# Kernel optimization log

Hardware: AMD Instinct MI355X
Metric: run time of the kernel (lower is better)

The kernel has to match this reference:

```python
import jax, jax.numpy as jnp
import numpy as np
import math

D_MODEL = 1024
D_STATE = 128
D_CONV = 4
EXPAND = 2
HEADDIM = 64
NGROUPS = 1
D_INNER = EXPAND * D_MODEL            # 2048
D_SSM = D_INNER                       # d_ssm defaults to d_inner
NHEADS = D_SSM // HEADDIM             # 32
CONV_DIM = D_SSM + 2 * NGROUPS * D_STATE   # 2304
D_IN_PROJ = 2 * D_INNER + 2 * NGROUPS * D_STATE + NHEADS  # 4384
EPS = 1e-5
DT_MIN, DT_MAX = 1e-3, 1e-1


def setup_inputs() -> dict:
    key = jax.random.key(0)
    ks = jax.random.split(key, 8)
    u = jax.random.normal(ks[0], (2, 4096, D_MODEL), dtype=jnp.float32)
    W_in = jax.random.normal(ks[1], (D_IN_PROJ, D_MODEL), dtype=jnp.float32) * 0.02
    conv_w = jax.random.normal(ks[2], (CONV_DIM, D_CONV), dtype=jnp.float32) * 0.1
    conv_b = jnp.zeros((CONV_DIM,), dtype=jnp.float32)
    # dt_bias init as in the module: inv-softplus of dt ~ logU(dt_min, dt_max)
    dt = jnp.exp(jax.random.uniform(ks[3], (NHEADS,)) * (math.log(DT_MAX) - math.log(DT_MIN)) + math.log(DT_MIN))
    dt_bias = dt + jnp.log(-jnp.expm1(-dt))
    A_log = jnp.log(jax.random.uniform(ks[4], (NHEADS,), minval=1.0, maxval=16.0))
    D = jnp.ones((NHEADS,), dtype=jnp.float32)
    norm_w = jnp.ones((D_SSM,), dtype=jnp.float32)
    W_out = jax.random.normal(ks[5], (D_MODEL, D_INNER), dtype=jnp.float32) * 0.02
    return {"u": u, "W_in": W_in, "conv_w": conv_w, "conv_b": conv_b,
            "dt_bias": dt_bias, "A_log": A_log, "D": D, "norm_w": norm_w, "W_out": W_out}


def _mamba2_forward(u, W_in, conv_w, conv_b, dt_bias, A_log, D, norm_w, W_out):
    b, L, _ = u.shape
    zxbcdt = jnp.einsum('bld,ed->ble', u, W_in)  # (b, L, D_IN_PROJ)
    z = zxbcdt[..., :D_SSM]
    xBC = zxbcdt[..., D_SSM:D_SSM + CONV_DIM]
    dt = zxbcdt[..., D_SSM + CONV_DIM:]                     # (b, L, H)
    dt = jax.nn.softplus(dt + dt_bias)                      # (b, L, H)

    # causal depthwise conv1d + SiLU (channel-last, kernel width D_CONV)
    xp = jnp.pad(xBC, ((0, 0), (D_CONV - 1, 0), (0, 0)))
    conv = conv_b
    for w in range(D_CONV):
        conv = conv + xp[:, w:w + L, :] * conv_w[:, w]
    xBC = jax.nn.silu(conv)

    x = xBC[..., :D_SSM].reshape(b, L, NHEADS, HEADDIM)     # (b, L, H, P)
    B = xBC[..., D_SSM:D_SSM + D_STATE]                     # (b, L, N), ngroups=1
    C = xBC[..., D_SSM + D_STATE:]                          # (b, L, N)

    A = -jnp.exp(A_log)                                     # (H,)
    dA = jnp.exp(dt * A)                                    # (b, L, H)
    dtx = dt[..., None] * x                                 # (b, L, H, P)

    # selective state-space scan over time: h_t = h_{t-1}*dA_t + dt_t*x_t (x) B_t
    def step(h, inp):
        dA_t, dtx_t, B_t, C_t = inp                        # (b,H), (b,H,P), (b,N), (b,N)
        h = h * dA_t[:, :, None, None] + jnp.einsum('bhp,bn->bhpn', dtx_t, B_t)
        y_t = jnp.einsum('bhpn,bn->bhp', h, C_t)
        return h, y_t

    h0 = jnp.zeros((b, NHEADS, HEADDIM, D_STATE), dtype=u.dtype)
    inputs = (jnp.moveaxis(dA, 1, 0), jnp.moveaxis(dtx, 1, 0),
              jnp.moveaxis(B, 1, 0), jnp.moveaxis(C, 1, 0))
    _, y = jax.lax.scan(step, h0, inputs)                   # (L, b, H, P)
    y = jnp.moveaxis(y, 0, 1) + x * D[None, None, :, None]  # D skip per head
    y = y.reshape(b, L, D_SSM)

    # gated RMSNorm (norm_before_gate=False): normalize(y * silu(z)) * weight
    g = y * jax.nn.silu(z)
    g = g * jax.lax.rsqrt(jnp.mean(g * g, axis=-1, keepdims=True) + EPS) * norm_w
    return jnp.einsum('ble,de->bld', g, W_out)              # (b, L, D_MODEL)


def reference(u, W_in, conv_w, conv_b, dt_bias, A_log, D, norm_w, W_out):
    return _mamba2_forward(u, W_in, conv_w, conv_b, dt_bias, A_log, D, norm_w, W_out)
```

## Files before the change

### kernel.cpp

```cpp
#include <hip/hip_runtime.h>
#include <hip/hip_bf16.h>
#include <cstdint>

#define BB     2
#define LSEQ   4096
#define DM     1024
#define DSSM   2048
#define NH     32
#define HD     64
#define DS     128
#define NPROJ  4384
#define NPAD   4480
#define CONVD  2304
#define ROWS   (BB*LSEQ)
#define CHUNK  128
#define NCH    (LSEQ/CHUNK)
#define NBHC   (BB*NH*NCH)

typedef __bf16 bf16x8 __attribute__((ext_vector_type(8)));
typedef float  f32x4  __attribute__((ext_vector_type(4)));
typedef float  f32x16 __attribute__((ext_vector_type(16)));

__device__ __forceinline__ __bf16 to_bf(float f) {
    __hip_bfloat16 h = __float2bfloat16(f);
    return *(__bf16*)&h;
}

__device__ __forceinline__ void direct_load16(const void* gp, void* lp) {
    typedef const __attribute__((address_space(1))) unsigned int* gptr_t;
    typedef __attribute__((address_space(3))) unsigned int* lptr_t;
    __builtin_amdgcn_global_load_lds((gptr_t)(uintptr_t)gp,
                                     (lptr_t)(unsigned int)(uintptr_t)lp,
                                     16, 0, 0);
}

#define N1 ((size_t)ROWS * DM)
#define N2 ((size_t)NPAD * DM)
#define N3 ((size_t)DM * DSSM)
#define NREAL ((size_t)NPROJ * DM)

__global__ __launch_bounds__(256) void convert_all(const float* __restrict__ u,
                                                   const float* __restrict__ W_in,
                                                   const float* __restrict__ W_out,
                                                   __hip_bfloat16* __restrict__ ub,
                                                   __hip_bfloat16* __restrict__ winb,
                                                   __hip_bfloat16* __restrict__ woutb) {
    size_t i4 = ((size_t)blockIdx.x * 256 + threadIdx.x) * 4;
    const float* src;
    __hip_bfloat16* dst;
    size_t j;
    if (i4 < N1) { src = u; dst = ub; j = i4; }
    else if (i4 < N1 + N2) {
        j = i4 - N1;
        if (j >= NREAL) {
            ushort4 z = {0, 0, 0, 0};
            *(ushort4*)&winb[j] = z;
            return;
        }
        src = W_in; dst = winb;
    } else { src = W_out; dst = woutb; j = i4 - N1 - N2; }
    float4 v = *(const float4*)&src[j];
    __hip_bfloat16 o[4] = {__float2bfloat16(v.x), __float2bfloat16(v.y),
                           __float2bfloat16(v.z), __float2bfloat16(v.w)};
    *(ushort4*)&dst[j] = *(ushort4*)o;
}

__device__ __forceinline__ void storeC(float v, float* p) { *p = v; }
__device__ __forceinline__ void storeC(float v, __hip_bfloat16* p) { *p = __float2bfloat16(v); }

template <typename CT>
__global__ __launch_bounds__(256) void gemm_bt(const __hip_bfloat16* __restrict__ A,
                                               const __hip_bfloat16* __restrict__ B,
                                               CT* __restrict__ C,
                                               int M, int N, int K, int lda, int ldc) {
    __shared__ __bf16 lA[128 * 32];
    __shared__ __bf16 lB[128 * 32];
    const int tid = threadIdx.x;
    const int wv = tid >> 6, ln = tid & 63;

    const int gridM = M >> 7, gridN = N >> 7;
    const int pid = blockIdx.x;
    const int gsize = 8 * gridN;
    const int g = pid / gsize;
    const int first_m = g * 8;
    const int sz = min(8, gridM - first_m);
    const int m0 = (first_m + (pid % gsize) % sz) * 128;
    const int n0 = ((pid % gsize) / sz) * 128;

    const int wrow = (wv >> 1) * 64, wcol = (wv & 1) * 64;
    const int l31 = ln & 31, khalf = ln >> 5;
    const int sw = (l31 >> 2) & 3;

    f32x16 acc[2][2] = {};

    const int scol = (((ln & 3) ^ ((ln >> 4) & 3))) * 8;
    const int sr0 = wv * 16 + (ln >> 2);
    const int sr1 = (4 + wv) * 16 + (ln >> 2);

    const __hip_bfloat16* Ab = A + (size_t)m0 * lda;
    const __hip_bfloat16* Bb = B + (size_t)n0 * K;

    for (int k0 = 0; k0 < K; k0 += 32) {
        direct_load16(Ab + (size_t)sr0 * lda + k0 + scol, &lA[(size_t)wv * 512]);
        direct_load16(Ab + (size_t)sr1 * lda + k0 + scol, &lA[(size_t)(4 + wv) * 512]);
        direct_load16(Bb + (size_t)sr0 * K + k0 + scol, &lB[(size_t)wv * 512]);
        direct_load16(Bb + (size_t)sr1 * K + k0 + scol, &lB[(size_t)(4 + wv) * 512]);
        __syncthreads();

        #pragma unroll
        for (int ks = 0; ks < 2; ++ks) {
            const int ce = ((ks * 2 + khalf) ^ sw) * 8;
            bf16x8 af[2], bfr[2];
            #pragma unroll
            for (int tm = 0; tm < 2; ++tm)
                af[tm]  = *(const bf16x8*)&lA[(wrow + tm * 32 + l31) * 32 + ce];
            #pragma unroll
            for (int tn = 0; tn < 2; ++tn)
                bfr[tn] = *(const bf16x8*)&lB[(wcol + tn * 32 + l31) * 32 + ce];
            #pragma unroll
            for (int tm = 0; tm < 2; ++tm)
                #pragma unroll
                for (int tn = 0; tn < 2; ++tn)
                    acc[tm][tn] = __builtin_amdgcn_mfma_f32_32x32x16_bf16(af[tm], bfr[tn], acc[tm][tn], 0, 0, 0);
        }
        __syncthreads();
    }

    #pragma unroll
    for (int tm = 0; tm < 2; ++tm) {
        #pragma unroll
        for (int tn = 0; tn < 2; ++tn) {
            const int rbase = m0 + wrow + tm * 32 + 4 * khalf;
            const int c0 = n0 + wcol + tn * 32 + l31;
            #pragma unroll
            for (int r = 0; r < 16; ++r) {
                const int row = rbase + (r & 3) + 8 * (r >> 2);
                storeC(acc[tm][tn][r], &C[(size_t)row * ldc + c0]);
            }
        }
    }
}

__global__ __launch_bounds__(256) void conv_fused(const __hip_bfloat16* __restrict__ zx,
                                                  const float* __restrict__ conv_w,
                                                  const float* __restrict__ conv_b,
                                                  const float* __restrict__ dt_bias,
                                                  __hip_bfloat16* __restrict__ xT,
                                                  __hip_bfloat16* __restrict__ Bv,
                                                  __hip_bfloat16* __restrict__ Cv,
                                                  __hip_bfloat16* __restrict__ BT,
                                                  float* __restrict__ dtv) {
    const int ct = blockIdx.x;
    const int rb = blockIdx.y * 64;
    const int tid = threadIdx.x;
    const int b = rb >> 12, l0 = rb & (LSEQ - 1);

    if (ct == 36) {
        const int r = tid >> 2, h8 = (tid & 3) * 8;
        const int gr = rb + r;
        bf16x8 v8 = *(const bf16x8*)&zx[(size_t)gr * NPAD + DSSM + CONVD + h8];
        float o[8];
        #pragma unroll
        for (int j = 0; j < 8; ++j) {
            float v = (float)v8[j] + dt_bias[h8 + j];
            o[j] = (v > 20.f) ? v : log1pf(__expf(v));
        }
        *(float4*)&dtv[(size_t)gr * NH + h8]     = *(float4*)&o[0];
        *(float4*)&dtv[(size_t)gr * NH + h8 + 4] = *(float4*)&o[4];
        return;
    }

    __shared__ __bf16 t[64][72];
    const int c0 = ct * 64;
    const int sc = (tid & 7) * 8;
    const int r2 = (tid >> 3) * 2;
    const int gc = c0 + sc;

    float cb[8];
    *(float4*)&cb[0] = *(const float4*)&conv_b[gc];
    *(float4*)&cb[4] = *(const float4*)&conv_b[gc + 4];
    float4 cw[8];
    #pragma unroll
    for (int j = 0; j < 8; ++j) cw[j] = *(const float4*)&conv_w[(gc + j) * 4];

    float in[5][8];
    #pragma unroll
    for (int i = 0; i < 5; ++i) {
        int ll = l0 + r2 - 3 + i;
        if (ll >= 0) {
            bf16x8 v = *(const bf16x8*)&zx[(size_t)(b * LSEQ + ll) * NPAD + DSSM + gc];
            #pragma unroll
            for (int j = 0; j < 8; ++j) in[i][j] = (float)v[j];
        } else {
            #pragma unroll
            for (int j = 0; j < 8; ++j) in[i][j] = 0.f;
        }
    }

    bf16x8 o0, o1;
    #pragma unroll
    for (int j = 0; j < 8; ++j) {
        float a0 = cb[j] + cw[j].x * in[0][j] + cw[j].y * in[1][j] + cw[j].z * in[2][j] + cw[j].w * in[3][j];
        float a1 = cb[j] + cw[j].x * in[1][j] + cw[j].y * in[2][j] + cw[j].z * in[3][j] + cw[j].w * in[4][j];
        o0[j] = to_bf(a0 / (1.f + __expf(-a0)));
        o1[j] = to_bf(a1 / (1.f + __expf(-a1)));
    }

    if (ct >= 32 && ct < 34) {
        const int bc = gc - 2048;
        *(bf16x8*)&Bv[(size_t)(rb + r2) * DS + bc]     = o0;
        *(bf16x8*)&Bv[(size_t)(rb + r2 + 1) * DS + bc] = o1;
    } else if (ct >= 34) {
        const int cc = gc - 2176;
        *(bf16x8*)&Cv[(size_t)(rb + r2) * DS + cc]     = o0;
        *(bf16x8*)&Cv[(size_t)(rb + r2 + 1) * DS + cc] = o1;
    }

    if (ct < 34) {
        #pragma unroll
        for (int j = 0; j < 8; ++j) { t[sc + j][r2] = o0[j]; t[sc + j][r2 + 1] = o1[j]; }
        __syncthreads();
        const int trow = tid >> 3, tcolg = (tid & 7) * 8;
        #pragma unroll
        for (int hfl = 0; hfl < 2; ++hfl) {
            const int rr = hfl * 32 + trow;
            bf16x8 o;
            #pragma unroll
            for (int j = 0; j < 8; ++j) o[j] = t[rr][tcolg + j];
            __hip_bfloat16* dst = (ct < 32)
                ? &xT[(size_t)(b * DSSM + c0 + rr) * LSEQ + l0 + tcolg]
                : &BT[(size_t)(b * DS + (c0 - 2048) + rr) * LSEQ + l0 + tcolg];
            *(bf16x8*)dst = o;
        }
    }
}

__global__ __launch_bounds__(256) void chunk_local(const __hip_bfloat16* __restrict__ xT,
                                                   const __hip_bfloat16* __restrict__ BT,
                                                   const float* __restrict__ dtv,
                                                   const float* __restrict__ A_log,
                                                   __hip_bfloat16* __restrict__ sst,
                                                   float* __restrict__ lcg) {
    __shared__ __bf16 lXT[4][HD * 32];
    __shared__ __bf16 lBT[4][DS * 32];
    __shared__ float sc[2][CHUNK];
    __shared__ float lw[CHUNK];

    const int bid = blockIdx.x;
    const int c = bid & 31, hh = (bid >> 5) & 31, b = bid >> 10;
    const int tid = threadIdx.x;
    const int wv = tid >> 6, ln = tid & 63;
    const int r0 = b * LSEQ + c * CHUNK;
    const int s0 = c * CHUNK;

    {
        const int row16 = ln >> 2, col8 = (ln & 3) * 8;
        const __hip_bfloat16* Bb = BT + (size_t)b * DS * LSEQ + s0 + wv * 32 + col8;
        #pragma unroll
        for (int j = 0; j < 8; ++j)
            direct_load16(Bb + (size_t)(j * 16 + row16) * LSEQ, &lBT[wv][j * 512]);
    }

    float dt_s = 0.f;
    if (tid < CHUNK) {
        dt_s = dtv[(size_t)(r0 + tid) * NH + hh];
        sc[0][tid] = -__expf(A_log[hh]) * dt_s;
    }
    __syncthreads();
    int src = 0;
    for (int off = 1; off < CHUNK; off <<= 1) {
        if (tid < CHUNK)
            sc[src ^ 1][tid] = sc[src][tid] + ((tid >= off) ? sc[src][tid - off] : 0.f);
        __syncthreads();
        src ^= 1;
    }
    if (tid < CHUNK) {
        float Lc = sc[src][tid];
        lcg[(size_t)bid * CHUNK + tid] = Lc;
        lw[tid] = dt_s * __expf(sc[src][CHUNK - 1] - Lc);
    }
    __syncthreads();

    {
        const int p = tid >> 2, ks = tid & 3;
        const __hip_bfloat16* xr = xT + (size_t)(b * DSSM + hh * HD + p) * LSEQ + s0 + ks * 32;
        #pragma unroll
        for (int v = 0; v < 4; ++v) {
            bf16x8 xv = *(const bf16x8*)&xr[v * 8];
            float4 w0 = *(const float4*)&lw[ks * 32 + v * 8];
            float4 w1 = *(const float4*)&lw[ks * 32 + v * 8 + 4];
            bf16x8 o;
            o[0] = to_bf((float)xv[0] * w0.x); o[1] = to_bf((float)xv[1] * w0.y);
            o[2] = to_bf((float)xv[2] * w0.z); o[3] = to_bf((float)xv[3] * w0.w);
            o[4] = to_bf((float)xv[4] * w1.x); o[5] = to_bf((float)xv[5] * w1.y);
            o[6] = to_bf((float)xv[6] * w1.z); o[7] = to_bf((float)xv[7] * w1.w);
            *(bf16x8*)&lXT[ks][p * 32 + v * 8] = o;
        }
    }
    __syncthreads();

    const int lane15 = ln & 15, quad = ln >> 4;
    f32x4 acc[4][2] = {};
    #pragma unroll
    for (int ks = 0; ks < 4; ++ks) {
        bf16x8 af[4], bf[2];
        #pragma unroll
        for (int mi = 0; mi < 4; ++mi)
            af[mi] = *(const bf16x8*)&lXT[ks][(mi * 16 + lane15) * 32 + quad * 8];
        #pragma unroll
        for (int ni = 0; ni < 2; ++ni)
            bf[ni] = *(const bf16x8*)&lBT[ks][(wv * 32 + ni * 16 + lane15) * 32 + quad * 8];
        #pragma unroll
        for (int mi = 0; mi < 4; ++mi)
            #pragma unroll
            for (int ni = 0; ni < 2; ++ni)
                acc[mi][ni] = __builtin_amdgcn_mfma_f32_16x16x32_bf16(af[mi], bf[ni], acc[mi][ni], 0, 0, 0);
    }

    __hip_bfloat16* sb = sst + (size_t)bid * (HD * DS);
    #pragma unroll
    for (int mi = 0; mi < 4; ++mi)
        #pragma unroll
        for (int ni = 0; ni < 2; ++ni) {
            int p0 = mi * 16 + quad * 4;
            int n0 = wv * 32 + ni * 16 + lane15;
            #pragma unroll
            for (int r = 0; r < 4; ++r)
                sb[(size_t)(p0 + r) * DS + n0] = __float2bfloat16(acc[mi][ni][r]);
        }
}

__global__ __launch_bounds__(256) void chunk_scan(__hip_bfloat16* __restrict__ sst,
                                                  const float* __restrict__ lcg) {
    const int bid = blockIdx.x;
    const int bh = bid >> 5;
    const int elem = (bid & 31) * 256 + threadIdx.x;
    float h = 0.f;
    size_t base = (size_t)bh * NCH * (HD * DS) + elem;
    const float* lg = lcg + (size_t)bh * NCH * CHUNK;
    for (int cc = 0; cc < NCH; ++cc) {
        float cq = __expf(lg[cc * CHUNK + CHUNK - 1]);
        size_t a = base + (size_t)cc * (HD * DS);
        float sv = __bfloat162float(sst[a]);
        sst[a] = __float2bfloat16(h);
        h = cq * h + sv;
    }
}

__global__ __launch_bounds__(256) void chunk_y(const __hip_bfloat16* __restrict__ xT,
                                               const __hip_bfloat16* __restrict__ Bv,
                                               const __hip_bfloat16* __restrict__ Cv,
                                               const float* __restrict__ dtv,
                                               const float* __restrict__ lcg,
                                               const __hip_bfloat16* __restrict__ sst,
                                               const float* __restrict__ Dv,
                                               __hip_bfloat16* __restrict__ y) {
    __shared__ __bf16 lC[4][128 * 32];
    __shared__ __bf16 lB[4][128 * 32];

    const int bid = blockIdx.x;
    const int c = bid & 31, hh = (bid >> 5) & 31, b = bid >> 10;
    const int tid = threadIdx.x;
    const int wv = tid >> 6, ln = tid & 63;
    const int lane15 = ln & 15, quad = ln >> 4;
    const int r0 = b * LSEQ + c * CHUNK;

    const __hip_bfloat16* Cb = Cv + (size_t)r0 * DS;
    const __hip_bfloat16* Bb = Bv + (size_t)r0 * DS;
    const __hip_bfloat16* Hb = sst + (size_t)bid * (HD * DS);
    const float* lg = lcg + (size_t)bid * CHUNK;

    {
        const int i3 = ln & 3, i4 = ln >> 2;
        #pragma unroll
        for (int j = 0; j < 8; ++j) {
            direct_load16(Cb + (size_t)(j * 16 + i4) * DS + wv * 32 + i3 * 8, &lC[wv][j * 512]);
            direct_load16(Bb + (size_t)(j * 16 + i4) * DS + wv * 32 + i3 * 8, &lB[wv][j * 512]);
        }
    }
    __syncthreads();

    const int wrow = (wv >> 1) * 64, wcol = (wv & 1) * 64;
    const int wr2 = wv * 32;
    f32x4 acc[4][4] = {};
    f32x4 accY[2][4] = {};

    #pragma unroll
    for (int ks = 0; ks < 4; ++ks) {
        bf16x8 af[4], bfr[4], af2[2], bh[4];
        #pragma unroll
        for (int i = 0; i < 4; ++i) {
            af[i]  = *(const bf16x8*)&lC[ks][(wrow + i * 16 + lane15) * 32 + quad * 8];
            bfr[i] = *(const bf16x8*)&lB[ks][(wcol + i * 16 + lane15) * 32 + quad * 8];
        }
        #pragma unroll
        for (int mi = 0; mi < 2; ++mi)
            af2[mi] = *(const bf16x8*)&lC[ks][(wr2 + mi * 16 + lane15) * 32 + quad * 8];
        #pragma unroll
        for (int ni = 0; ni < 4; ++ni)
            bh[ni] = *(const bf16x8*)&Hb[(size_t)(ni * 16 + lane15) * DS + ks * 32 + quad * 8];
        #pragma unroll
        for (int mi = 0; mi < 4; ++mi)
            #pragma unroll
            for (int ni = 0; ni < 4; ++ni)
                acc[mi][ni] = __builtin_amdgcn_mfma_f32_16x16x32_bf16(af[mi], bfr[ni], acc[mi][ni], 0, 0, 0);
        #pragma unroll
        for (int mi = 0; mi < 2; ++mi)
            #pragma unroll
            for (int ni = 0; ni < 4; ++ni)
                accY[mi][ni] = __builtin_amdgcn_mfma_f32_16x16x32_bf16(af2[mi], bh[ni], accY[mi][ni], 0, 0, 0);
    }

    #pragma unroll
    for (int mi = 0; mi < 2; ++mi)
        #pragma unroll
        for (int r = 0; r < 4; ++r) {
            float cum = __expf(lg[wr2 + mi * 16 + quad * 4 + r]);
            #pragma unroll
            for (int ni = 0; ni < 4; ++ni) accY[mi][ni][r] *= cum;
        }

    float Lct[16];
    #pragma unroll
    for (int mi = 0; mi < 4; ++mi)
        #pragma unroll
        for (int r = 0; r < 4; ++r)
            Lct[mi * 4 + r] = lg[wrow + mi * 16 + quad * 4 + r];

    __syncthreads();

    {
        const int row16 = ln >> 2, col8 = (ln & 3) * 8;
        const __hip_bfloat16* xr = xT + (size_t)(b * DSSM + hh * HD) * LSEQ + c * CHUNK + wv * 32 + col8;
        #pragma unroll
        for (int j = 0; j < 4; ++j)
            direct_load16(xr + (size_t)(j * 16 + row16) * LSEQ, &lB[wv][j * 512]);
    }

    #pragma unroll
    for (int ni = 0; ni < 4; ++ni) {
        const int s = wcol + ni * 16 + lane15;
        const float Lcs = lg[s];
        const float dts = dtv[(size_t)(r0 + s) * NH + hh];
        #pragma unroll
        for (int mi = 0; mi < 4; ++mi) {
            #pragma unroll
            for (int r = 0; r < 4; ++r) {
                const int t = wrow + mi * 16 + quad * 4 + r;
                float v = (s <= t) ? acc[mi][ni][r] * __expf(Lct[mi * 4 + r] - Lcs) * dts : 0.f;
                lC[s >> 5][t * 32 + (s & 31)] = to_bf(v);
            }
        }
    }
    __syncthreads();

    #pragma unroll
    for (int ks = 0; ks < 4; ++ks) {
        bf16x8 af2[2], bx[4];
        #pragma unroll
        for (int mi = 0; mi < 2; ++mi)
            af2[mi] = *(const bf16x8*)&lC[ks][(wr2 + mi * 16 + lane15) * 32 + quad * 8];
        #pragma unroll
        for (int ni = 0; ni < 4; ++ni)
            bx[ni] = *(const bf16x8*)&lB[ks][(ni * 16 + lane15) * 32 + quad * 8];
        #pragma unroll
        for (int mi = 0; mi < 2; ++mi)
            #pragma unroll
            for (int ni = 0; ni < 4; ++ni)
                accY[mi][ni] = __builtin_amdgcn_mfma_f32_16x16x32_bf16(af2[mi], bx[ni], accY[mi][ni], 0, 0, 0);
    }

    const float dsc = Dv[hh];
    #pragma unroll
    for (int mi = 0; mi < 2; ++mi)
        #pragma unroll
        for (int ni = 0; ni < 4; ++ni) {
            const int p0 = ni * 16 + lane15;
            #pragma unroll
            for (int r = 0; r < 4; ++r) {
                const int t = wr2 + mi * 16 + quad * 4 + r;
                accY[mi][ni][r] += dsc * (float)lB[t >> 5][p0 * 32 + (t & 31)];
            }
        }

    __hip_bfloat16* yb = y + (size_t)r0 * DSSM + hh * HD;
    #pragma unroll
    for (int mi = 0; mi < 2; ++mi)
        #pragma unroll
        for (int ni = 0; ni < 4; ++ni) {
            const int p0 = ni * 16 + lane15;
            #pragma unroll
            for (int r = 0; r < 4; ++r) {
                const int t = wr2 + mi * 16 + quad * 4 + r;
                yb[(size_t)t * DSSM + p0] = __float2bfloat16(accY[mi][ni][r]);
            }
        }
}

__global__ __launch_bounds__(256) void gnorm_kernel(const __hip_bfloat16* __restrict__ y,
                                                    __hip_bfloat16* __restrict__ zx,
                                                    const float* __restrict__ nw) {
    const int r = blockIdx.x;
    const int tid = threadIdx.x;
    const int c = tid * 8;
    const size_t off = (size_t)r * DSSM + c;
    bf16x8 yv8 = *(const bf16x8*)&y[off];
    bf16x8 zv8 = *(const bf16x8*)&zx[(size_t)r * NPAD + c];
    float gv[8];
    float ss = 0.f;
    #pragma unroll
    for (int i = 0; i < 8; ++i) {
        float yv = (float)yv8[i];
        float z = (float)zv8[i];
        float gq = yv * (z / (1.f + __expf(-z)));
        gv[i] = gq;
        ss += gq * gq;
    }
    #pragma unroll
    for (int o = 32; o; o >>= 1) ss += __shfl_xor(ss, o, 64);
    __shared__ float ws4[4];
    if ((tid & 63) == 0) ws4[tid >> 6] = ss;
    __syncthreads();
    const float tot = ws4[0] + ws4[1] + ws4[2] + ws4[3];
    const float scale = rsqrtf(tot * (1.f / (float)DSSM) + 1e-5f);
    bf16x8 o;
    #pragma unroll
    for (int i = 0; i < 8; ++i) o[i] = to_bf(gv[i] * scale * nw[c + i]);
    *(bf16x8*)&zx[(size_t)r * NPAD + DSSM + c] = o;
}

extern "C" void kernel_launch(void* const* d_in, const int* in_sizes, int n_in,
                              void* d_out, int out_size, void* d_ws, size_t ws_size,
                              hipStream_t stream) {
    const float* u       = (const float*)d_in[0];
    const float* W_in    = (const float*)d_in[1];
    const float* conv_w  = (const float*)d_in[2];
    const float* conv_b  = (const float*)d_in[3];
    const float* dt_bias = (const float*)d_in[4];
    const float* A_log   = (const float*)d_in[5];
    const float* Dv      = (const float*)d_in[6];
    const float* norm_w  = (const float*)d_in[7];
    const float* W_out   = (const float*)d_in[8];
    float* out = (float*)d_out;

    char* ws = (char*)d_ws;
    size_t off = 0;
    auto alloc = [&](size_t bytes) { char* p = ws + off; off += (bytes + 255) & ~(size_t)255; return p; };

    __hip_bfloat16* ub    = (__hip_bfloat16*)alloc((size_t)ROWS * DM * 2);
    __hip_bfloat16* winb  = (__hip_bfloat16*)alloc((size_t)NPAD * DM * 2);
    __hip_bfloat16* woutb = (__hip_bfloat16*)alloc((size_t)DM * DSSM * 2);
    __hip_bfloat16* zx    = (__hip_bfloat16*)alloc((size_t)ROWS * NPAD * 2);
    __hip_bfloat16* yb    = (__hip_bfloat16*)alloc((size_t)ROWS * DSSM * 2);
    __hip_bfloat16* sst   = (__hip_bfloat16*)alloc((size_t)NBHC * HD * DS * 2);
    __hip_bfloat16* xT    = (__hip_bfloat16*)alloc((size_t)ROWS * DSSM * 2);
    __hip_bfloat16* BT    = (__hip_bfloat16*)alloc((size_t)ROWS * DS * 2);

    __hip_bfloat16* Bvp = (__hip_bfloat16*)ub;
    __hip_bfloat16* Cvp = Bvp + (size_t)ROWS * DS;
    float*          dtv = (float*)(Cvp + (size_t)ROWS * DS);
    float*          lcg = (float*)winb;

    convert_all<<<(unsigned)((N1 + N2 + N3) / 4 / 256), 256, 0, stream>>>(
        u, W_in, W_out, ub, winb, woutb);

    gemm_bt<__hip_bfloat16><<<(ROWS / 128) * (NPAD / 128), 256, 0, stream>>>(
        ub, winb, zx, ROWS, NPAD, DM, DM, NPAD);

    conv_fused<<<dim3(37, ROWS / 64), 256, 0, stream>>>(
        zx, conv_w, conv_b, dt_bias, xT, Bvp, Cvp, BT, dtv);

    chunk_local<<<NBHC, 256, 0, stream>>>(xT, BT, dtv, A_log, sst, lcg);
    chunk_scan<<<NBHC, 256, 0, stream>>>(sst, lcg);
    chunk_y<<<NBHC, 256, 0, stream>>>(xT, Bvp, Cvp, dtv, lcg, sst, Dv, yb);

    gnorm_kernel<<<ROWS, 256, 0, stream>>>(yb, zx, norm_w);

    gemm_bt<float><<<(ROWS / 128) * (DM / 128), 256, 0, stream>>>(
        zx + DSSM, woutb, out, ROWS, DM, DSSM, NPAD, DM);
}
```

Baseline: 377.3 us.

## Double-buffer GEMM LDS tiles and vectorize chunk_y score writes

The bf16 GEMM now ping-pongs between two LDS buffers, so the direct global-to-LDS loads for the next K-slice are issued before the MFMA work on the current slice. This is meant to overlap memory latency with compute, at the cost of doubling the shared memory per block. In chunk_y, the cumulative log-decay and dt values are staged in LDS. The C·B score product is transposed by swapping operands, so each lane writes four contiguous bf16 values as one vector store instead of four scattered scalar stores.

```diff
diff --git a/kernel.cpp b/kernel.cpp
--- a/kernel.cpp
+++ b/kernel.cpp
@@ -18,6 +18,7 @@
 #define NBHC   (BB*NH*NCH)
 
 typedef __bf16 bf16x8 __attribute__((ext_vector_type(8)));
+typedef __bf16 bf16x4v __attribute__((ext_vector_type(4)));
 typedef float  f32x4  __attribute__((ext_vector_type(4)));
 typedef float  f32x16 __attribute__((ext_vector_type(16)));
 
@@ -73,8 +74,8 @@
                                                const __hip_bfloat16* __restrict__ B,
                                                CT* __restrict__ C,
                                                int M, int N, int K, int lda, int ldc) {
-    __shared__ __bf16 lA[128 * 32];
-    __shared__ __bf16 lB[128 * 32];
+    __shared__ __bf16 lA[2][128 * 32];
+    __shared__ __bf16 lB[2][128 * 32];
     const int tid = threadIdx.x;
     const int wv = tid >> 6, ln = tid & 63;
 
@@ -100,30 +101,40 @@
     const __hip_bfloat16* Ab = A + (size_t)m0 * lda;
     const __hip_bfloat16* Bb = B + (size_t)n0 * K;
 
-    for (int k0 = 0; k0 < K; k0 += 32) {
-        direct_load16(Ab + (size_t)sr0 * lda + k0 + scol, &lA[(size_t)wv * 512]);
-        direct_load16(Ab + (size_t)sr1 * lda + k0 + scol, &lA[(size_t)(4 + wv) * 512]);
-        direct_load16(Bb + (size_t)sr0 * K + k0 + scol, &lB[(size_t)wv * 512]);
-        direct_load16(Bb + (size_t)sr1 * K + k0 + scol, &lB[(size_t)(4 + wv) * 512]);
-        __syncthreads();
-
+    auto issue = [&](int buf, int k0) {
+        direct_load16(Ab + (size_t)sr0 * lda + k0 + scol, &lA[buf][wv * 512]);
+        direct_load16(Ab + (size_t)sr1 * lda + k0 + scol, &lA[buf][(4 + wv) * 512]);
+        direct_load16(Bb + (size_t)sr0 * K + k0 + scol, &lB[buf][wv * 512]);
+        direct_load16(Bb + (size_t)sr1 * K + k0 + scol, &lB[buf][(4 + wv) * 512]);
+    };
+    auto compute = [&](int buf) {
         #pragma unroll
         for (int ks = 0; ks < 2; ++ks) {
             const int ce = ((ks * 2 + khalf) ^ sw) * 8;
             bf16x8 af[2], bfr[2];
             #pragma unroll
             for (int tm = 0; tm < 2; ++tm)
-                af[tm]  = *(const bf16x8*)&lA[(wrow + tm * 32 + l31) * 32 + ce];
+                af[tm]  = *(const bf16x8*)&lA[buf][(wrow + tm * 32 + l31) * 32 + ce];
             #pragma unroll
             for (int tn = 0; tn < 2; ++tn)
-                bfr[tn] = *(const bf16x8*)&lB[(wcol + tn * 32 + l31) * 32 + ce];
+                bfr[tn] = *(const bf16x8*)&lB[buf][(wcol + tn * 32 + l31) * 32 + ce];
             #pragma unroll
             for (int tm = 0; tm < 2; ++tm)
                 #pragma unroll
                 for (int tn = 0; tn < 2; ++tn)
                     acc[tm][tn] = __builtin_amdgcn_mfma_f32_32x32x16_bf16(af[tm], bfr[tn], acc[tm][tn], 0, 0, 0);
         }
+    };
+
+    issue(0, 0);
+    const int nb = K / 32;
+    for (int it = 0; it < nb; it += 2) {
         __syncthreads();
+        if (it + 1 < nb) issue(1, (it + 1) * 32);
+        compute(0);
+        __syncthreads();
+        if (it + 2 < nb) issue(0, (it + 2) * 32);
+        compute(1);
     }
 
     #pragma unroll
@@ -357,6 +368,8 @@
                                                __hip_bfloat16* __restrict__ y) {
     __shared__ __bf16 lC[4][128 * 32];
     __shared__ __bf16 lB[4][128 * 32];
+    __shared__ float sLc[CHUNK];
+    __shared__ float sdt[CHUNK];
 
     const int bid = blockIdx.x;
     const int c = bid & 31, hh = (bid >> 5) & 31, b = bid >> 10;
@@ -368,7 +381,6 @@
     const __hip_bfloat16* Cb = Cv + (size_t)r0 * DS;
     const __hip_bfloat16* Bb = Bv + (size_t)r0 * DS;
     const __hip_bfloat16* Hb = sst + (size_t)bid * (HD * DS);
-    const float* lg = lcg + (size_t)bid * CHUNK;
 
     {
         const int i3 = ln & 3, i4 = ln >> 2;
@@ -377,6 +389,10 @@
             direct_load16(Cb + (size_t)(j * 16 + i4) * DS + wv * 32 + i3 * 8, &lC[wv][j * 512]);
             direct_load16(Bb + (size_t)(j * 16 + i4) * DS + wv * 32 + i3 * 8, &lB[wv][j * 512]);
         }
+    }
+    if (tid < CHUNK) {
+        sLc[tid] = lcg[(size_t)bid * CHUNK + tid];
+        sdt[tid] = dtv[(size_t)(r0 + tid) * NH + hh];
     }
     __syncthreads();
 
@@ -390,8 +406,8 @@
         bf16x8 af[4], bfr[4], af2[2], bh[4];
         #pragma unroll
         for (int i = 0; i < 4; ++i) {
-            af[i]  = *(const bf16x8*)&lC[ks][(wrow + i * 16 + lane15) * 32 + quad * 8];
-            bfr[i] = *(const bf16x8*)&lB[ks][(wcol + i * 16 + lane15) * 32 + quad * 8];
+            af[i]  = *(const bf16x8*)&lB[ks][(wrow + i * 16 + lane15) * 32 + quad * 8];
+            bfr[i] = *(const bf16x8*)&lC[ks][(wcol + i * 16 + lane15) * 32 + quad * 8];
         }
         #pragma unroll
         for (int mi = 0; mi < 2; ++mi)
@@ -415,17 +431,10 @@
     for (int mi = 0; mi < 2; ++mi)
         #pragma unroll
         for (int r = 0; r < 4; ++r) {
-            float cum = __expf(lg[wr2 + mi * 16 + quad * 4 + r]);
+            float cum = __expf(sLc[wr2 + mi * 16 + quad * 4 + r]);
             #pragma unroll
             for (int ni = 0; ni < 4; ++ni) accY[mi][ni][r] *= cum;
         }
-
-    float Lct[16];
-    #pragma unroll
-    for (int mi = 0; mi < 4; ++mi)
-        #pragma unroll
-        for (int r = 0; r < 4; ++r)
-            Lct[mi * 4 + r] = lg[wrow + mi * 16 + quad * 4 + r];
 
     __syncthreads();
 
@@ -438,18 +447,23 @@
     }
 
     #pragma unroll
-    for (int ni = 0; ni < 4; ++ni) {
-        const int s = wcol + ni * 16 + lane15;
-        const float Lcs = lg[s];
-        const float dts = dtv[(size_t)(r0 + s) * NH + hh];
-        #pragma unroll
-        for (int mi = 0; mi < 4; ++mi) {
+    for (int mi = 0; mi < 4; ++mi) {
+        const int sb = wrow + mi * 16 + quad * 4;
+        float el[4], dt4[4];
+        #pragma unroll
+        for (int r = 0; r < 4; ++r) { el[r] = sLc[sb + r]; dt4[r] = sdt[sb + r]; }
+        #pragma unroll
+        for (int ni = 0; ni < 4; ++ni) {
+            const int t = wcol + ni * 16 + lane15;
+            const float Lct = sLc[t];
+            bf16x4v o;
             #pragma unroll
             for (int r = 0; r < 4; ++r) {
-                const int t = wrow + mi * 16 + quad * 4 + r;
-                float v = (s <= t) ? acc[mi][ni][r] * __expf(Lct[mi * 4 + r] - Lcs) * dts : 0.f;
-                lC[s >> 5][t * 32 + (s & 31)] = to_bf(v);
+                const int s = sb + r;
+                float v = (s <= t) ? acc[mi][ni][r] * __expf(Lct - el[r]) * dt4[r] : 0.f;
+                o[r] = to_bf(v);
             }
+            *(bf16x4v*)&lC[sb >> 5][t * 32 + (sb & 31)] = o;
         }
     }
     __syncthreads();
```

New measurement: 377.4 us. Within noise of the previous version (+0.0%).
